# Kernel optimization log

Hardware: AMD Instinct MI355X
Metric: run time of the kernel (lower is better)

Reference implementation:

```python
import jax, jax.numpy as jnp
import numpy as np
import math

HIDDEN = 2048
N_HEADS = 16
HEAD = HIDDEN // N_HEADS
B, S = 2, 2048


def setup_inputs() -> dict:
    key = jax.random.key(0)
    k1, k2, k3 = jax.random.split(key, 3)
    scale = 1.0 / math.sqrt(HIDDEN)
    return {
        "x": jax.random.normal(k1, (B, S, HIDDEN), dtype=jnp.float32),
        "w_qkv": jax.random.normal(k2, (HIDDEN, 3 * HIDDEN), dtype=jnp.float32) * scale,
        "b_qkv": jnp.zeros((3 * HIDDEN,), dtype=jnp.float32),
        "w_out": jax.random.normal(k3, (HIDDEN, HIDDEN), dtype=jnp.float32) * scale,
        "b_out": jnp.zeros((HIDDEN,), dtype=jnp.float32),
    }


def reference(x, w_qkv, b_qkv, w_out, b_out):
    b, s, _ = x.shape
    qkv = x @ w_qkv + b_qkv                      # [b, s, 3*hidden]
    q, k, v = jnp.split(qkv, 3, axis=-1)
    # 'b n (h l) -> b h n l'
    def heads(t):
        return t.reshape(b, s, N_HEADS, HEAD).transpose(0, 2, 1, 3)
    q, k, v = heads(q), heads(k), heads(v)
    scores = jnp.einsum("bhql,bhkl->bhqk", q, k) / math.sqrt(HEAD)
    # causal mask: positions where q_ind < k_ind get -10000 (matches source)
    q_ind = jnp.arange(s)[:, None]
    k_ind = jnp.arange(s)[None, :]
    scores = jnp.where(q_ind < k_ind, jnp.float32(-10000.0), scores)
    probs = jax.nn.softmax(scores, axis=-1)
    combined = jnp.einsum("bhqk,bhkl->bhql", probs, v)
    # 'b h q l -> b q (h l)'
    combined = combined.transpose(0, 2, 1, 3).reshape(b, s, HIDDEN)
    return combined @ w_out + b_out
```

## Files before the change

### kernel.cpp

```cpp
#include <hip/hip_runtime.h>
#include <hip/hip_bf16.h>

typedef __attribute__((ext_vector_type(4))) float f32x4;
typedef __attribute__((ext_vector_type(16))) float f32x16;
typedef __attribute__((ext_vector_type(8))) short bf16x8;

#define GBL_AS(p) (const __attribute__((address_space(1))) void*)(p)
#define LDS_AS(p) (__attribute__((address_space(3))) void*)(p)

__device__ __forceinline__ void gload_lds16(const void* g, void* l) {
  __builtin_amdgcn_global_load_lds(GBL_AS(g), LDS_AS(l), 16, 0, 0);
}

__device__ __forceinline__ ushort f2bf(float f) {
  union { float f; unsigned int u; } v; v.f = f;
  unsigned int r = v.u + 0x7fffu + ((v.u >> 16) & 1u);
  return (ushort)(r >> 16);
}

__global__ void cast_f32_bf16_kernel(const float4* __restrict__ in,
                                     ushort4* __restrict__ out, int n4) {
  int i = blockIdx.x * 256 + threadIdx.x;
  if (i < n4) {
    float4 v = in[i];
    ushort4 o;
    o.x = f2bf(v.x); o.y = f2bf(v.y); o.z = f2bf(v.z); o.w = f2bf(v.w);
    out[i] = o;
  }
}

__global__ void transpose_cast_kernel(const float* __restrict__ in,
                                      ushort* __restrict__ out, int R, int C) {
  __shared__ float tile[64][65];
  int tx = threadIdx.x & 63, ty = threadIdx.x >> 6;
  int r0 = blockIdx.y * 64, c0 = blockIdx.x * 64;
#pragma unroll
  for (int i = 0; i < 64; i += 4)
    tile[ty + i][tx] = in[(size_t)(r0 + ty + i) * C + (c0 + tx)];
  __syncthreads();
#pragma unroll
  for (int i = 0; i < 64; i += 4)
    out[(size_t)(c0 + ty + i) * R + (r0 + tx)] = f2bf(tile[tx][ty + i]);
}

template <int MODE>
__global__ __launch_bounds__(256, 2) void gemm_bt_kernel(
    const ushort* __restrict__ A, const ushort* __restrict__ Bt,
    const float* __restrict__ bias, float* __restrict__ C,
    ushort* __restrict__ Qo, ushort* __restrict__ Ko, ushort* __restrict__ Vo,
    int M, int N, int K) {
  __shared__ ushort As[128 * 64];
  __shared__ ushort Bs[128 * 64];
  const int tid = threadIdx.x;
  const int w = tid >> 6, l = tid & 63;
  const int wr = w >> 1, wc = w & 1;
  const int m0 = blockIdx.y * 128, n0 = blockIdx.x * 128;

  f32x4 acc[4][4] = {};

  const int lr = l >> 3;
  const int lc = (l & 7) ^ lr;

  for (int k0 = 0; k0 < K; k0 += 64) {
#pragma unroll
    for (int i = 0; i < 4; ++i) {
      int row = i * 32 + w * 8 + lr;
      gload_lds16(A + (size_t)(m0 + row) * K + k0 + lc * 8,
                  (char*)As + (i * 32 + w * 8) * 128);
      gload_lds16(Bt + (size_t)(n0 + row) * K + k0 + lc * 8,
                  (char*)Bs + (i * 32 + w * 8) * 128);
    }
    __syncthreads();
    const char* Ab = (const char*)As;
    const char* Bb = (const char*)Bs;
#pragma unroll
    for (int ks = 0; ks < 2; ++ks) {
      bf16x8 af[4], bfr[4];
      int cc = ks * 4 + (l >> 4);
#pragma unroll
      for (int mi = 0; mi < 4; ++mi) {
        int row = wr * 64 + mi * 16 + (l & 15);
        af[mi] = *(const bf16x8*)(Ab + row * 128 + ((cc ^ (row & 7)) << 4));
      }
#pragma unroll
      for (int ni = 0; ni < 4; ++ni) {
        int row = wc * 64 + ni * 16 + (l & 15);
        bfr[ni] = *(const bf16x8*)(Bb + row * 128 + ((cc ^ (row & 7)) << 4));
      }
#pragma unroll
      for (int mi = 0; mi < 4; ++mi)
#pragma unroll
        for (int ni = 0; ni < 4; ++ni)
          acc[mi][ni] = __builtin_amdgcn_mfma_f32_16x16x32_bf16(
              af[mi], bfr[ni], acc[mi][ni], 0, 0, 0);
    }
    __syncthreads();
  }

  if (MODE == 0) {
#pragma unroll
    for (int mi = 0; mi < 4; ++mi) {
      int row = m0 + wr * 64 + mi * 16 + ((l >> 4) << 2);
#pragma unroll
      for (int ni = 0; ni < 4; ++ni) {
        int col = n0 + wc * 64 + ni * 16 + (l & 15);
        float b = bias[col];
#pragma unroll
        for (int r = 0; r < 4; ++r)
          C[(size_t)(row + r) * N + col] = acc[mi][ni][r] + b;
      }
    }
  } else {
    const float qscale = 0.08838834764831845f * 1.4426950408889634f;
#pragma unroll
    for (int ni = 0; ni < 4; ++ni) {
      int n = n0 + wc * 64 + ni * 16 + (l & 15);
      int which = n >> 11;
      int cc2 = n & 2047;
      int h = cc2 >> 7, d = cc2 & 127;
      float b = bias[n];
#pragma unroll
      for (int mi = 0; mi < 4; ++mi) {
        int m = m0 + wr * 64 + mi * 16 + ((l >> 4) << 2);
        int bb = m >> 11, s = m & 2047;
        int bh = bb * 16 + h;
        if (which == 0) {
#pragma unroll
          for (int r = 0; r < 4; ++r)
            Qo[((size_t)bh * 2048 + s + r) * 128 + d] =
                f2bf((acc[mi][ni][r] + b) * qscale);
        } else if (which == 1) {
#pragma unroll
          for (int r = 0; r < 4; ++r)
            Ko[((size_t)bh * 2048 + s + r) * 128 + d] = f2bf(acc[mi][ni][r] + b);
        } else {
          ushort4 pk;
          pk.x = f2bf(acc[mi][ni][0] + b);
          pk.y = f2bf(acc[mi][ni][1] + b);
          pk.z = f2bf(acc[mi][ni][2] + b);
          pk.w = f2bf(acc[mi][ni][3] + b);
          *(ushort4*)(Vo + ((size_t)bh * 128 + d) * 2048 + s) = pk;
        }
      }
    }
  }
}

__global__ __launch_bounds__(512, 2) void attn_kernel(
    const ushort* __restrict__ Qg, const ushort* __restrict__ Kg,
    const ushort* __restrict__ Vtg, ushort* __restrict__ Og) {
  constexpr int S = 2048, D = 128;
  __shared__ ushort Kl[2][64 * 128];

  const int tid = threadIdx.x, w = tid >> 6, l = tid & 63;
  const int lid = blockIdx.x;
  const int bh = lid & 31;
  const int j = lid >> 5;
  const int g = w >> 2, wv = w & 3;
  const int qb = (g == 0) ? (8 + j) : (7 - j);
  const int wq0 = qb * 128 + wv * 32;
  const int nt_blk = 18 + 2 * j;
  const int ql = l & 31, h32 = l >> 5;

  const ushort* Qb = Qg + (size_t)bh * S * D;
  const ushort* Kb = Kg + (size_t)bh * S * D;
  const ushort* Vb = Vtg + (size_t)bh * D * S;

  bf16x8 qf[8];
#pragma unroll
  for (int ks = 0; ks < 8; ++ks)
    qf[ks] = *(const bf16x8*)(Qb + (size_t)(wq0 + ql) * D + ks * 16 + h32 * 8);

  f32x16 o[4];
#pragma unroll
  for (int dt = 0; dt < 4; ++dt) o[dt] = 0.f;
  float mrun = -1e30f, lrun = 0.f;

  auto stage = [&](int t, int buf) {
    const int k0 = t * 64;
#pragma unroll
    for (int s2 = 0; s2 < 2; ++s2) {
      int i = w * 2 + s2;
      int row = i * 4 + (l >> 4);
      int ck = (l & 15) ^ (row & 7);
      gload_lds16(Kb + (size_t)(k0 + row) * D + ck * 8,
                  (char*)Kl[buf] + i * 1024);
    }
  };

  stage(0, 0);

  for (int t = 0; t < nt_blk; ++t) {
    const int cur = t & 1;
    const int k0 = t * 64;
    if (t + 1 < nt_blk) {
      stage(t + 1, cur ^ 1);
      asm volatile("s_waitcnt vmcnt(2)" ::: "memory");
    } else {
      asm volatile("s_waitcnt vmcnt(0)" ::: "memory");
    }
    __builtin_amdgcn_s_barrier();

    if (k0 < wq0 + 32) {
      const char* Kc = (const char*)Kl[cur];

      bf16x8 kf0[8], kf1[8];
      {
        const int swz0 = ql & 7;
        const char* base0 = Kc + ql * 256;
        const char* base1 = Kc + (32 + ql) * 256;
#pragma unroll
        for (int ks = 0; ks < 8; ++ks) {
          int c = 2 * ks + h32;
          kf0[ks] = *(const bf16x8*)(base0 + ((c ^ swz0) << 4));
          kf1[ks] = *(const bf16x8*)(base1 + ((c ^ swz0) << 4));
        }
      }
      f32x16 sa[2];
      sa[0] = 0.f; sa[1] = 0.f;
      __builtin_amdgcn_s_setprio(1);
#pragma unroll
      for (int ks = 0; ks < 8; ++ks) {
        sa[0] = __builtin_amdgcn_mfma_f32_32x32x16_bf16(kf0[ks], qf[ks], sa[0],
                                                        0, 0, 0);
        sa[1] = __builtin_amdgcn_mfma_f32_32x32x16_bf16(kf1[ks], qf[ks], sa[1],
                                                        0, 0, 0);
      }
      __builtin_amdgcn_s_setprio(0);

      bf16x8 vf[2][2][4];
      {
        const ushort* vrow = Vb + (size_t)ql * S + k0;
#pragma unroll
        for (int kt = 0; kt < 2; ++kt)
#pragma unroll
          for (int u2 = 0; u2 < 2; ++u2) {
            int c = 4 * kt + 2 * u2 + h32;
#pragma unroll
            for (int dt = 0; dt < 4; ++dt)
              vf[kt][u2][dt] =
                  *(const bf16x8*)(vrow + (size_t)dt * 32 * S + c * 8);
          }
      }

      if (k0 + 63 > wq0) {
        int qq = wq0 + ql;
#pragma unroll
        for (int kt = 0; kt < 2; ++kt) {
          int kb = k0 + kt * 32 + 4 * h32;
#pragma unroll
          for (int rr = 0; rr < 16; ++rr) {
            int kk = kb + (rr & 3) + 8 * (rr >> 2);
            if (qq < kk) sa[kt][rr] = -1e9f;
          }
        }
      }

      float tmax = -1e30f;
#pragma unroll
      for (int kt = 0; kt < 2; ++kt)
#pragma unroll
        for (int rr = 0; rr < 16; ++rr) tmax = fmaxf(tmax, sa[kt][rr]);
      tmax = fmaxf(tmax, __shfl_xor(tmax, 32));

      if (!__all(tmax <= mrun + 11.5f)) {
        float mnew = fmaxf(mrun, tmax);
        float e = __builtin_amdgcn_exp2f(mrun - mnew);
        lrun *= e;
        mrun = mnew;
#pragma unroll
        for (int dt = 0; dt < 4; ++dt) o[dt] *= e;
      }

      float rsum = 0.f;
#pragma unroll
      for (int kt = 0; kt < 2; ++kt)
#pragma unroll
        for (int rr = 0; rr < 16; ++rr) {
          float p = __builtin_amdgcn_exp2f(sa[kt][rr] - mrun);
          sa[kt][rr] = p;
          rsum += p;
        }
      rsum += __shfl_xor(rsum, 32);
      lrun += rsum;

#pragma unroll
      for (int kt = 0; kt < 2; ++kt) {
#pragma unroll
        for (int u2 = 0; u2 < 2; ++u2) {
          int A0, B0, A1, B1;
          asm("v_cvt_pk_bf16_f32 %0, %1, %2"
              : "=v"(A0) : "v"(sa[kt][u2 * 8 + 0]), "v"(sa[kt][u2 * 8 + 1]));
          asm("v_cvt_pk_bf16_f32 %0, %1, %2"
              : "=v"(B0) : "v"(sa[kt][u2 * 8 + 2]), "v"(sa[kt][u2 * 8 + 3]));
          asm("v_cvt_pk_bf16_f32 %0, %1, %2"
              : "=v"(A1) : "v"(sa[kt][u2 * 8 + 4]), "v"(sa[kt][u2 * 8 + 5]));
          asm("v_cvt_pk_bf16_f32 %0, %1, %2"
              : "=v"(B1) : "v"(sa[kt][u2 * 8 + 6]), "v"(sa[kt][u2 * 8 + 7]));
          auto r02 = __builtin_amdgcn_permlane32_swap(A0, A1, false, false);
          auto r13 = __builtin_amdgcn_permlane32_swap(B0, B1, false, false);
          union { int i[4]; bf16x8 v; } pu;
          pu.i[0] = r02[0];
          pu.i[1] = r13[0];
          pu.i[2] = r02[1];
          pu.i[3] = r13[1];
          __builtin_amdgcn_s_setprio(1);
#pragma unroll
          for (int dt = 0; dt < 4; ++dt)
            o[dt] = __builtin_amdgcn_mfma_f32_32x32x16_bf16(
                vf[kt][u2][dt], pu.v, o[dt], 0, 0, 0);
          __builtin_amdgcn_s_setprio(0);
        }
      }
    }
    asm volatile("s_waitcnt lgkmcnt(0)" ::: "memory");
    __builtin_amdgcn_s_barrier();
  }

  const int b = bh >> 4, h = bh & 15;
  float inv = 1.0f / lrun;
  size_t rowbase = ((size_t)b * 2048 + (wq0 + ql)) * 2048 + h * 128;
#pragma unroll
  for (int dt = 0; dt < 4; ++dt)
#pragma unroll
    for (int r4 = 0; r4 < 4; ++r4) {
      int col = dt * 32 + r4 * 8 + h32 * 4;
      ushort4 pk;
      pk.x = f2bf(o[dt][r4 * 4 + 0] * inv);
      pk.y = f2bf(o[dt][r4 * 4 + 1] * inv);
      pk.z = f2bf(o[dt][r4 * 4 + 2] * inv);
      pk.w = f2bf(o[dt][r4 * 4 + 3] * inv);
      *(ushort4*)(Og + rowbase + col) = pk;
    }
}

extern "C" void kernel_launch(void* const* d_in, const int* in_sizes, int n_in,
                              void* d_out, int out_size, void* d_ws,
                              size_t ws_size, hipStream_t stream) {
  const float* x = (const float*)d_in[0];
  const float* w_qkv = (const float*)d_in[1];
  const float* b_qkv = (const float*)d_in[2];
  const float* w_out = (const float*)d_in[3];
  const float* b_out = (const float*)d_in[4];
  float* out = (float*)d_out;
  char* ws = (char*)d_ws;

  if (ws_size < 92274688u) return;
  ushort* xb = (ushort*)(ws);
  ushort* wqkvt = (ushort*)(ws + 16777216);
  ushort* Q = (ushort*)(ws + 41943040);
  ushort* Kb = (ushort*)(ws + 58720256);
  ushort* Vt = (ushort*)(ws + 75497472);
  ushort* comb = xb;
  ushort* woutt = wqkvt;

  cast_f32_bf16_kernel<<<8192, 256, 0, stream>>>((const float4*)x, (ushort4*)xb,
                                                 2097152);
  transpose_cast_kernel<<<dim3(96, 32), 256, 0, stream>>>(w_qkv, wqkvt, 2048,
                                                          6144);
  gemm_bt_kernel<1><<<dim3(48, 32), 256, 0, stream>>>(
      xb, wqkvt, b_qkv, nullptr, Q, Kb, Vt, 4096, 6144, 2048);
  transpose_cast_kernel<<<dim3(32, 32), 256, 0, stream>>>(w_out, woutt, 2048,
                                                          2048);
  attn_kernel<<<dim3(256), 512, 0, stream>>>(Q, Kb, Vt, comb);
  gemm_bt_kernel<0><<<dim3(16, 32), 256, 0, stream>>>(
      comb, woutt, b_out, out, nullptr, nullptr, nullptr, 4096, 2048, 2048);
}
```

Before: 261.2 us.

## Stage V tiles in LDS and double the attention key tile to 128

```diff
diff --git a/kernel.cpp b/kernel.cpp
--- a/kernel.cpp
+++ b/kernel.cpp
@@ -150,7 +150,8 @@
     const ushort* __restrict__ Qg, const ushort* __restrict__ Kg,
     const ushort* __restrict__ Vtg, ushort* __restrict__ Og) {
   constexpr int S = 2048, D = 128;
-  __shared__ ushort Kl[2][64 * 128];
+  __shared__ ushort Kl[2][128 * 128];
+  __shared__ ushort Vl[2][128 * 128];
 
   const int tid = threadIdx.x, w = tid >> 6, l = tid & 63;
   const int lid = blockIdx.x;
@@ -159,7 +160,7 @@
   const int g = w >> 2, wv = w & 3;
   const int qb = (g == 0) ? (8 + j) : (7 - j);
   const int wq0 = qb * 128 + wv * 32;
-  const int nt_blk = 18 + 2 * j;
+  const int nt_blk = 9 + j;
   const int ql = l & 31, h32 = l >> 5;
 
   const ushort* Qb = Qg + (size_t)bh * S * D;
@@ -177,25 +178,33 @@
   float mrun = -1e30f, lrun = 0.f;
 
   auto stage = [&](int t, int buf) {
-    const int k0 = t * 64;
-#pragma unroll
-    for (int s2 = 0; s2 < 2; ++s2) {
-      int i = w * 2 + s2;
+    const int k0 = t * 128;
+#pragma unroll
+    for (int s2 = 0; s2 < 4; ++s2) {
+      int i = w * 4 + s2;
       int row = i * 4 + (l >> 4);
       int ck = (l & 15) ^ (row & 7);
       gload_lds16(Kb + (size_t)(k0 + row) * D + ck * 8,
                   (char*)Kl[buf] + i * 1024);
     }
+#pragma unroll
+    for (int s2 = 0; s2 < 4; ++s2) {
+      int i = w * 4 + s2;
+      int row = i * 4 + (l >> 4);
+      int ck = (l & 15) ^ (row & 7);
+      gload_lds16(Vb + (size_t)row * S + k0 + ck * 8,
+                  (char*)Vl[buf] + i * 1024);
+    }
   };
 
   stage(0, 0);
 
   for (int t = 0; t < nt_blk; ++t) {
     const int cur = t & 1;
-    const int k0 = t * 64;
+    const int k0 = t * 128;
     if (t + 1 < nt_blk) {
       stage(t + 1, cur ^ 1);
-      asm volatile("s_waitcnt vmcnt(2)" ::: "memory");
+      asm volatile("s_waitcnt vmcnt(8)" ::: "memory");
     } else {
       asm volatile("s_waitcnt vmcnt(0)" ::: "memory");
     }
@@ -203,50 +212,38 @@
 
     if (k0 < wq0 + 32) {
       const char* Kc = (const char*)Kl[cur];
-
-      bf16x8 kf0[8], kf1[8];
-      {
-        const int swz0 = ql & 7;
-        const char* base0 = Kc + ql * 256;
-        const char* base1 = Kc + (32 + ql) * 256;
+      const char* Vc = (const char*)Vl[cur];
+      const int swz0 = ql & 7;
+
+      f32x16 sa[4];
+#pragma unroll
+      for (int kt = 0; kt < 4; ++kt) sa[kt] = 0.f;
+#pragma unroll
+      for (int p = 0; p < 2; ++p) {
+        bf16x8 kf0[8], kf1[8];
+        const char* base0 = Kc + (p * 64 + ql) * 256;
+        const char* base1 = Kc + (p * 64 + 32 + ql) * 256;
 #pragma unroll
         for (int ks = 0; ks < 8; ++ks) {
           int c = 2 * ks + h32;
           kf0[ks] = *(const bf16x8*)(base0 + ((c ^ swz0) << 4));
           kf1[ks] = *(const bf16x8*)(base1 + ((c ^ swz0) << 4));
         }
-      }
-      f32x16 sa[2];
-      sa[0] = 0.f; sa[1] = 0.f;
-      __builtin_amdgcn_s_setprio(1);
-#pragma unroll
-      for (int ks = 0; ks < 8; ++ks) {
-        sa[0] = __builtin_amdgcn_mfma_f32_32x32x16_bf16(kf0[ks], qf[ks], sa[0],
-                                                        0, 0, 0);
-        sa[1] = __builtin_amdgcn_mfma_f32_32x32x16_bf16(kf1[ks], qf[ks], sa[1],
-                                                        0, 0, 0);
-      }
-      __builtin_amdgcn_s_setprio(0);
-
-      bf16x8 vf[2][2][4];
-      {
-        const ushort* vrow = Vb + (size_t)ql * S + k0;
-#pragma unroll
-        for (int kt = 0; kt < 2; ++kt)
-#pragma unroll
-          for (int u2 = 0; u2 < 2; ++u2) {
-            int c = 4 * kt + 2 * u2 + h32;
-#pragma unroll
-            for (int dt = 0; dt < 4; ++dt)
-              vf[kt][u2][dt] =
-                  *(const bf16x8*)(vrow + (size_t)dt * 32 * S + c * 8);
-          }
-      }
-
-      if (k0 + 63 > wq0) {
+        __builtin_amdgcn_s_setprio(1);
+#pragma unroll
+        for (int ks = 0; ks < 8; ++ks) {
+          sa[p * 2] = __builtin_amdgcn_mfma_f32_32x32x16_bf16(
+              kf0[ks], qf[ks], sa[p * 2], 0, 0, 0);
+          sa[p * 2 + 1] = __builtin_amdgcn_mfma_f32_32x32x16_bf16(
+              kf1[ks], qf[ks], sa[p * 2 + 1], 0, 0, 0);
+        }
+        __builtin_amdgcn_s_setprio(0);
+      }
+
+      if (k0 + 127 > wq0) {
         int qq = wq0 + ql;
 #pragma unroll
-        for (int kt = 0; kt < 2; ++kt) {
+        for (int kt = 0; kt < 4; ++kt) {
           int kb = k0 + kt * 32 + 4 * h32;
 #pragma unroll
           for (int rr = 0; rr < 16; ++rr) {
@@ -258,7 +255,7 @@
 
       float tmax = -1e30f;
 #pragma unroll
-      for (int kt = 0; kt < 2; ++kt)
+      for (int kt = 0; kt < 4; ++kt)
 #pragma unroll
         for (int rr = 0; rr < 16; ++rr) tmax = fmaxf(tmax, sa[kt][rr]);
       tmax = fmaxf(tmax, __shfl_xor(tmax, 32));
@@ -274,7 +271,7 @@
 
       float rsum = 0.f;
 #pragma unroll
-      for (int kt = 0; kt < 2; ++kt)
+      for (int kt = 0; kt < 4; ++kt)
 #pragma unroll
         for (int rr = 0; rr < 16; ++rr) {
           float p = __builtin_amdgcn_exp2f(sa[kt][rr] - mrun);
@@ -285,9 +282,16 @@
       lrun += rsum;
 
 #pragma unroll
-      for (int kt = 0; kt < 2; ++kt) {
+      for (int kt = 0; kt < 4; ++kt) {
 #pragma unroll
         for (int u2 = 0; u2 < 2; ++u2) {
+          int c = 4 * kt + 2 * u2 + h32;
+          bf16x8 vf[4];
+#pragma unroll
+          for (int dt = 0; dt < 4; ++dt) {
+            int row = dt * 32 + ql;
+            vf[dt] = *(const bf16x8*)(Vc + row * 256 + ((c ^ swz0) << 4));
+          }
           int A0, B0, A1, B1;
           asm("v_cvt_pk_bf16_f32 %0, %1, %2"
               : "=v"(A0) : "v"(sa[kt][u2 * 8 + 0]), "v"(sa[kt][u2 * 8 + 1]));
@@ -307,8 +311,8 @@
           __builtin_amdgcn_s_setprio(1);
 #pragma unroll
           for (int dt = 0; dt < 4; ++dt)
-            o[dt] = __builtin_amdgcn_mfma_f32_32x32x16_bf16(
-                vf[kt][u2][dt], pu.v, o[dt], 0, 0, 0);
+            o[dt] = __builtin_amdgcn_mfma_f32_32x32x16_bf16(vf[dt], pu.v, o[dt],
+                                                            0, 0, 0);
           __builtin_amdgcn_s_setprio(0);
         }
       }
```

Result: faster. 223.3 us (-14.5%).
